# Kernel optimization log

Measured on AMD Instinct MI355X. Metric: run time of the kernel, lower is better.

The kernel has to match this reference:

```python
import jax, jax.numpy as jnp
import numpy as np


def setup_inputs() -> dict:
    key = jax.random.key(0)
    k1, k2, k3, k4 = jax.random.split(key, 4)
    b, N, c, h, w = 8, 150, 256, 128, 128
    mask_embed = jax.random.normal(k1, (b, N, c), dtype=jnp.float32)
    mask_features = jax.random.normal(k2, (b, c, h, w), dtype=jnp.float32)
    # Linear weights, torch convention: y = x @ W.T, std=0.02 trunc-normal-ish
    W_cls = jax.random.normal(k3, (c, c), dtype=jnp.float32) * 0.02
    W_feat = jax.random.normal(k4, (c, c), dtype=jnp.float32) * 0.02
    return {"mask_embed": mask_embed, "mask_features": mask_features,
            "W_cls": W_cls, "W_feat": W_feat}


def reference(mask_embed, mask_features, W_cls, W_feat):
    b, c, h, w = mask_features.shape
    cls_repr = mask_embed                                  # [b, N, c]
    img_feat = jnp.transpose(mask_features, (0, 2, 3, 1)).reshape(b, h * w, c)  # [b, hw, c]
    # coupled_attn: [b, N, hw]
    coupled_attn = jnp.einsum('bpc,bnc->bnp', img_feat, cls_repr)
    # class-direction softmax over pixels (dim=2)
    cls_attn = jax.nn.softmax(coupled_attn, axis=2)        # [b, N, hw]
    cls_offset = jnp.einsum('bnp,bpc->bnc', cls_attn, img_feat) @ W_cls.T
    aligned_cls_repr = cls_repr + cls_offset               # [b, N, c]
    # pixel-direction softmax over classes (dim=1)
    pos_attn = jax.nn.softmax(coupled_attn, axis=1)        # [b, N, hw]
    feat_offset = jnp.einsum('bnp,bnc->bpc', pos_attn, cls_repr) @ W_feat.T
    aligned_img_feat = img_feat + feat_offset              # [b, hw, c]
    aligned_img_feat = jnp.transpose(aligned_img_feat, (0, 2, 1)).reshape(b, c, h, w)
    return aligned_cls_repr, aligned_img_feat
```

## Files before the change

kernel.cpp:

```cpp
#include <hip/hip_runtime.h>

typedef unsigned short u16;
typedef __attribute__((ext_vector_type(8))) _Float16 f16x8;
typedef __attribute__((ext_vector_type(2))) _Float16 f16x2;
typedef __attribute__((ext_vector_type(4))) float f32x4;
typedef __attribute__((ext_vector_type(4))) unsigned short u16x4;
typedef __attribute__((ext_vector_type(8))) unsigned short u16x8;

#define MFMA16F __builtin_amdgcn_mfma_f32_16x16x32_f16

#define HW   16384
#define NCLS 150
#define NPAD 160
#define CDIM 256

#define FT_STRIDE 264
#define KC_STRIDE 72
#define FN_STRIDE 72
#define EP_STRIDE 72
#define W_STRIDE  168
#define CT_STRIDE 264

#define SO_FT   0
#define SO_CK   33792
#define SO_ROWM 56832
#define SO_ROWS 59392
#define SO_PMX  61952
#define SO_PZS  62464
#define SO_RZ   62976
#define SO_LDS  63232

#define O0_LDS  (NPAD*EP_STRIDE*2 + 128*FN_STRIDE*2)

#define WS_CLSF  0
#define WS_CLSWT 655360
#define WS_MG    2359296
#define WS_RZ    2364416
#define WS_WCF   2369536
#define WS_COMBT 2500608
#define WS_ROWP  3155968
#define WS_PART  3155968
#define WS_S     24127488

__device__ __forceinline__ u16 f2h(float f){ return __builtin_bit_cast(u16, (_Float16)f); }
__device__ __forceinline__ float h2f(u16 h){ return (float)__builtin_bit_cast(_Float16, h); }
__device__ __forceinline__ f16x2 shfl_h2(f16x2 v, int m){
  int x = __builtin_bit_cast(int, v);
  x = __shfl_xor(x, m);
  return __builtin_bit_cast(f16x2, x);
}

__global__ __launch_bounds__(256) void k0(const float* __restrict__ cls, const float* __restrict__ Wf,
                                          const float* __restrict__ Wc,
                                          u16* __restrict__ clsF, u16* __restrict__ clsWT,
                                          u16* __restrict__ WcF){
  int t = threadIdx.x;
  if (blockIdx.x >= 8*NPAD){
    int i = ((blockIdx.x - 8*NPAD)*256 + t)*4;
    f32x4 v = *(const f32x4*)&Wc[i];
    u16x4 o = {f2h(v[0]), f2h(v[1]), f2h(v[2]), f2h(v[3])};
    *(u16x4*)&WcF[i] = o;
    return;
  }
  int b = blockIdx.x / NPAD, n = blockIdx.x % NPAD;
  __shared__ float row[256];
  int bn = b*NPAD + n;
  if (n < NCLS){
    float v = cls[(b*NCLS + n)*CDIM + t];
    clsF[bn*CDIM + t] = f2h(v);
    row[t] = v;
    __syncthreads();
    float acc = 0.f;
    const float* wr = Wf + t*CDIM;
    #pragma unroll 4
    for (int c = 0; c < 256; c += 4){
      acc += row[c]*wr[c] + row[c+1]*wr[c+1] + row[c+2]*wr[c+2] + row[c+3]*wr[c+3];
    }
    clsWT[(b*CDIM + t)*NPAD + n] = f2h(acc);
  } else {
    clsF[bn*CDIM + t] = 0;
    clsWT[(b*CDIM + t)*NPAD + n] = 0;
  }
}

__global__ __launch_bounds__(512) void kSO1(const float* __restrict__ feat,
                                            const u16* __restrict__ clsF,
                                            const u16* __restrict__ clsWT,
                                            u16* __restrict__ Sg, float* __restrict__ rowP,
                                            float* __restrict__ out1){
  extern __shared__ char sm[];
  u16*  ftF  = (u16*)(sm + SO_FT);
  u16*  clsK = (u16*)(sm + SO_CK);
  u16*  E    = (u16*)(sm + SO_CK);
  float* rowM = (float*)(sm + SO_ROWM);
  float* rowS = (float*)(sm + SO_ROWS);
  float* pmx  = (float*)(sm + SO_PMX);
  float* pzs  = (float*)(sm + SO_PZS);
  float* rzL  = (float*)(sm + SO_RZ);

  int b = blockIdx.x & 7, tl = blockIdx.x >> 3, t = threadIdx.x;
  int p0 = tl*64;
  const float* featG = feat + (size_t)b*CDIM*HW;
  const u16* clsB  = clsF  + b*NPAD*CDIM;
  const u16* clsWB = clsWT + b*CDIM*NPAD;
  u16* Sb = Sg + (size_t)b*NPAD*HW;

  int lane = t & 63, wv = t >> 6;
  int l15 = lane & 15, lk = (lane >> 4) & 3;
  int nh = wv >> 2, pq = wv & 3;
  int nbase = nh*80;
  int col = pq*16 + l15;
  int cstrip = wv*32;

  {
    int p = t & 63, cg = t >> 6;
    #pragma unroll
    for (int i = 0; i < 8; ++i){
      int c0 = (i*8 + cg)*4;
      const float* g0 = featG + (size_t)c0*HW + p0 + p;
      float v0 = g0[0], v1 = g0[HW], v2 = g0[2*HW], v3 = g0[3*HW];
      u16x4 hv = {f2h(v0), f2h(v1), f2h(v2), f2h(v3)};
      *(u16x4*)&ftF[p*FT_STRIDE + c0] = hv;
    }
  }
  f32x4 acc[5];
  #pragma unroll
  for (int f = 0; f < 5; ++f) acc[f] = (f32x4){0.f,0.f,0.f,0.f};
  for (int kc = 0; kc < 4; ++kc){
    #pragma unroll
    for (int it = 0; it < 3; ++it){
      int idx = it*512 + t;
      if (idx < 1280){
        int n = idx >> 3, s8 = idx & 7;
        u16x8 v = *(const u16x8*)&clsB[n*CDIM + kc*64 + s8*8];
        *(u16x8*)&clsK[n*KC_STRIDE + s8*8] = v;
      }
    }
    __syncthreads();
    #pragma unroll
    for (int kb2 = 0; kb2 < 2; ++kb2){
      int kol = kb2*32 + lk*8;
      f16x8 bh = *(const f16x8*)&ftF[(pq*16 + l15)*FT_STRIDE + kc*64 + kol];
      #pragma unroll
      for (int f = 0; f < 5; ++f){
        f16x8 ah = *(const f16x8*)&clsK[(nbase + f*16 + l15)*KC_STRIDE + kol];
        acc[f] = MFMA16F(ah, bh, acc[f], 0, 0, 0);
      }
    }
    __syncthreads();
  }
  f16x8 aw0[5], aw1[5];
  #pragma unroll
  for (int kb = 0; kb < 5; ++kb){
    aw0[kb] = *(const f16x8*)&clsWB[(cstrip + l15)*NPAD + kb*32 + lk*8];
    aw1[kb] = *(const f16x8*)&clsWB[(cstrip + 16 + l15)*NPAD + kb*32 + lk*8];
  }
  #pragma unroll
  for (int kb = 0; kb < 5; ++kb){
    asm volatile("" :: "v"(aw0[kb]), "v"(aw1[kb]));
  }
  #pragma unroll
  for (int f = 0; f < 5; ++f){
    #pragma unroll
    for (int r = 0; r < 4; ++r){
      int n = nbase + f*16 + 4*lk + r;
      Sb[(size_t)n*HW + p0 + col] = f2h(acc[f][r]);
    }
  }
  #pragma unroll
  for (int f = 0; f < 5; ++f){
    #pragma unroll
    for (int rp = 0; rp < 2; ++rp){
      float v0 = acc[f][rp*2], v1 = acc[f][rp*2 + 1];
      f16x2 pm_ = {(_Float16)v0, (_Float16)v1};
      pm_ = __builtin_elementwise_max(pm_, shfl_h2(pm_, 1));
      pm_ = __builtin_elementwise_max(pm_, shfl_h2(pm_, 2));
      pm_ = __builtin_elementwise_max(pm_, shfl_h2(pm_, 4));
      pm_ = __builtin_elementwise_max(pm_, shfl_h2(pm_, 8));
      float m0 = (float)pm_[0], m1 = (float)pm_[1];
      f16x2 ps_ = {(_Float16)__expf(v0 - m0), (_Float16)__expf(v1 - m1)};
      ps_ = ps_ + shfl_h2(ps_, 1);
      ps_ = ps_ + shfl_h2(ps_, 2);
      ps_ = ps_ + shfl_h2(ps_, 4);
      ps_ = ps_ + shfl_h2(ps_, 8);
      if (l15 == f){
        int n0 = nbase + f*16 + 4*lk + rp*2;
        rowM[n0*4 + pq]       = m0;
        rowM[(n0 + 1)*4 + pq] = m1;
        rowS[n0*4 + pq]       = (float)ps_[0];
        rowS[(n0 + 1)*4 + pq] = (float)ps_[1];
      }
    }
  }
  {
    float pmax = -3.0e38f;
    #pragma unroll
    for (int f = 0; f < 5; ++f)
      #pragma unroll
      for (int r = 0; r < 4; ++r){
        int n = nbase + 16*f + 4*lk + r;
        if (n < NCLS) pmax = fmaxf(pmax, acc[f][r]);
      }
    pmax = fmaxf(pmax, __shfl_xor(pmax, 16));
    pmax = fmaxf(pmax, __shfl_xor(pmax, 32));
    if (lk == 0) pmx[nh*64 + col] = pmax;
  }
  __syncthreads();
  if (t < NPAD){
    float rm0 = rowM[t*4+0], rm1 = rowM[t*4+1], rm2 = rowM[t*4+2], rm3 = rowM[t*4+3];
    float msub = fmaxf(fmaxf(rm0, rm1), fmaxf(rm2, rm3));
    float l = rowS[t*4+0]*__expf(rm0 - msub) + rowS[t*4+1]*__expf(rm1 - msub)
            + rowS[t*4+2]*__expf(rm2 - msub) + rowS[t*4+3]*__expf(rm3 - msub);
    float* rp = rowP + ((size_t)(b*256 + tl)*NPAD + t)*2;
    rp[0] = msub;
    rp[1] = l;
  }
  {
    float mp_ = fmaxf(pmx[col], pmx[64 + col]);
    float s = 0.f;
    #pragma unroll
    for (int f = 0; f < 5; ++f){
      u16x4 ev;
      #pragma unroll
      for (int r = 0; r < 4; ++r){
        int n = nbase + 16*f + 4*lk + r;
        float e = (n < NCLS) ? __expf(acc[f][r] - mp_) : 0.f;
        s += e;
        ev[r] = f2h(e);
      }
      *(u16x4*)&E[col*W_STRIDE + nbase + 16*f + 4*lk] = ev;
    }
    s += __shfl_xor(s, 16);
    s += __shfl_xor(s, 32);
    if (lk == 0) pzs[nh*64 + col] = s;
  }
  __syncthreads();
  if (t < 64) rzL[t] = 1.0f / (pzs[t] + pzs[64 + t]);
  f32x4 accO[2][4];
  #pragma unroll
  for (int cf = 0; cf < 2; ++cf)
    #pragma unroll
    for (int pf = 0; pf < 4; ++pf) accO[cf][pf] = (f32x4){0.f,0.f,0.f,0.f};
  #pragma unroll
  for (int kb = 0; kb < 5; ++kb){
    int ko = kb*32 + lk*8;
    #pragma unroll
    for (int pf = 0; pf < 4; ++pf){
      f16x8 bb = *(const f16x8*)&E[(pf*16 + l15)*W_STRIDE + ko];
      accO[0][pf] = MFMA16F(aw0[kb], bb, accO[0][pf], 0, 0, 0);
      accO[1][pf] = MFMA16F(aw1[kb], bb, accO[1][pf], 0, 0, 0);
    }
  }
  __syncthreads();
  #pragma unroll
  for (int cf = 0; cf < 2; ++cf){
    #pragma unroll
    for (int r = 0; r < 4; ++r){
      int c = cstrip + cf*16 + lk*4 + r;
      float* ob = out1 + (size_t)(b*CDIM + c)*HW + p0;
      #pragma unroll
      for (int pf = 0; pf < 4; ++pf){
        int pp = pf*16 + l15;
        ob[pp] = accO[cf][pf][r]*rzL[pp] + h2f(ftF[pp*FT_STRIDE + c]);
      }
    }
  }
}

__global__ __launch_bounds__(256) void kComb(const float* __restrict__ rowP,
                                             float* __restrict__ mg, float* __restrict__ rz){
  int b = blockIdx.x / 10, nb = blockIdx.x % 10, t = threadIdx.x;
  int sg = t >> 4, j = t & 15;
  int n = nb*16 + j;
  __shared__ float pm[16][17], pl[16][17];
  float m = -3.0e38f, l = 0.f;
  for (int i = 0; i < 16; ++i){
    int s = sg*16 + i;
    const float* rp = rowP + ((size_t)(b*256 + s)*NPAD + n)*2;
    float ms = rp[0], ls = rp[1];
    float mn = fmaxf(m, ms);
    l = l*__expf(m - mn) + ls*__expf(ms - mn);
    m = mn;
  }
  pm[sg][j] = m;
  pl[sg][j] = l;
  __syncthreads();
  if (sg == 0){
    float M = pm[0][j], L = pl[0][j];
    #pragma unroll
    for (int k = 1; k < 16; ++k){
      float ms = pm[k][j], ls = pl[k][j];
      float mn = fmaxf(M, ms);
      L = L*__expf(M - mn) + ls*__expf(ms - mn);
      M = mn;
    }
    mg[b*NPAD + n] = M;
    rz[b*NPAD + n] = 1.0f / L;
  }
}

__global__ __launch_bounds__(512) void kOut0(const u16* __restrict__ Sg, const float* __restrict__ feat,
                                             const float* __restrict__ mg, u16* __restrict__ part){
  extern __shared__ char sm[];
  u16* Ep = (u16*)sm;
  u16* fN = (u16*)(sm + NPAD*EP_STRIDE*2);
  int b = blockIdx.x & 7, pr = (blockIdx.x >> 3) & 31, ch = (blockIdx.x >> 8) & 1;
  int t = threadIdx.x;
  const u16* Sb = Sg + (size_t)b*NPAD*HW;
  const float* featB = feat + (size_t)b*CDIM*HW;
  const float* mgB = mg + b*NPAD;
  int lane = t & 63, wv = t >> 6;
  int l15 = lane & 15, lk = (lane >> 4) & 3;
  int cstrip = wv*16;
  int rr = t >> 3, px8 = (t & 7)*8;
  f32x4 acc[10];
  #pragma unroll
  for (int nf = 0; nf < 10; ++nf) acc[nf] = (f32x4){0.f,0.f,0.f,0.f};
  for (int ck = 0; ck < 8; ++ck){
    int p0 = pr*512 + ck*64;
    #pragma unroll
    for (int ps = 0; ps < 3; ++ps){
      int rowi = ps*64 + rr;
      if (rowi < NPAD){
        u16x8 v = *(const u16x8*)&Sb[(size_t)rowi*HW + p0 + px8];
        float m = mgB[rowi];
        u16x8 o;
        #pragma unroll
        for (int j = 0; j < 8; ++j) o[j] = f2h(__expf(h2f(v[j]) - m));
        *(u16x8*)&Ep[rowi*EP_STRIDE + px8] = o;
      }
    }
    #pragma unroll
    for (int ps = 0; ps < 2; ++ps){
      int cl = ps*64 + rr;
      const float* g = featB + (size_t)(ch*128 + cl)*HW + p0 + px8;
      f32x4 v0 = *(const f32x4*)&g[0];
      f32x4 v1 = *(const f32x4*)&g[4];
      u16x8 o = {f2h(v0[0]), f2h(v0[1]), f2h(v0[2]), f2h(v0[3]),
                 f2h(v1[0]), f2h(v1[1]), f2h(v1[2]), f2h(v1[3])};
      *(u16x8*)&fN[cl*FN_STRIDE + px8] = o;
    }
    __syncthreads();
    #pragma unroll
    for (int kb = 0; kb < 2; ++kb){
      int ko = kb*32 + lk*8;
      f16x8 a0 = *(const f16x8*)&fN[(cstrip + l15)*FN_STRIDE + ko];
      #pragma unroll
      for (int nf = 0; nf < 10; ++nf){
        f16x8 bb = *(const f16x8*)&Ep[(nf*16 + l15)*EP_STRIDE + ko];
        acc[nf] = MFMA16F(a0, bb, acc[nf], 0, 0, 0);
      }
    }
    __syncthreads();
  }
  #pragma unroll
  for (int nf = 0; nf < 10; ++nf){
    #pragma unroll
    for (int r = 0; r < 4; ++r){
      int c = ch*128 + cstrip + lk*4 + r;
      int n = nf*16 + l15;
      part[((size_t)(b*32 + pr)*CDIM + c)*NPAD + n] = f2h(acc[nf][r]);
    }
  }
}

__global__ __launch_bounds__(256) void k4a(const u16* __restrict__ part, const float* __restrict__ rz,
                                           u16* __restrict__ combT){
  int b = blockIdx.x / 20, sub = blockIdx.x % 20, t = threadIdx.x;
  int idx8 = (sub*256 + t)*8;
  int c = idx8 / NPAD, n0 = idx8 % NPAD;
  const u16* base = part + (size_t)(b*32)*CDIM*NPAD + idx8;
  float a[8];
  #pragma unroll
  for (int j = 0; j < 8; ++j) a[j] = 0.f;
  for (int s = 0; s < 32; ++s){
    u16x8 v = *(const u16x8*)&base[(size_t)s*CDIM*NPAD];
    #pragma unroll
    for (int j = 0; j < 8; ++j) a[j] += h2f(v[j]);
  }
  const float* rzB = rz + b*NPAD + n0;
  #pragma unroll
  for (int j = 0; j < 8; ++j){
    combT[((size_t)(b*NPAD) + n0 + j)*CDIM + c] = f2h(a[j] * rzB[j]);
  }
}

__global__ __launch_bounds__(512) void k4b(const u16* __restrict__ combT, const u16* __restrict__ WcF,
                                           const float* __restrict__ cls, float* __restrict__ out0){
  extern __shared__ char sm[];
  u16* A = (u16*)sm;
  int b = blockIdx.x >> 1, nb = blockIdx.x & 1, t = threadIdx.x;
  const u16* cb = combT + (size_t)(b*NPAD + nb*80)*CDIM;
  #pragma unroll
  for (int it = 0; it < 10; ++it){
    int idx8 = (it*512 + t)*8;
    if (idx8 < 80*256){
      int row = idx8 >> 8, k0 = idx8 & 255;
      u16x8 v = *(const u16x8*)&cb[idx8];
      *(u16x8*)&A[row*CT_STRIDE + k0] = v;
    }
  }
  __syncthreads();
  int lane = t & 63, wv = t >> 6;
  int l15 = lane & 15, lk = (lane >> 4) & 3;
  int cstrip = wv*32;
  f32x4 acc[5][2];
  #pragma unroll
  for (int f = 0; f < 5; ++f)
    #pragma unroll
    for (int ct = 0; ct < 2; ++ct) acc[f][ct] = (f32x4){0.f,0.f,0.f,0.f};
  #pragma unroll
  for (int kb = 0; kb < 8; ++kb){
    int ko = kb*32 + lk*8;
    f16x8 b0 = *(const f16x8*)&WcF[(cstrip + l15)*CDIM + ko];
    f16x8 b1 = *(const f16x8*)&WcF[(cstrip + 16 + l15)*CDIM + ko];
    #pragma unroll
    for (int f = 0; f < 5; ++f){
      f16x8 af = *(const f16x8*)&A[(f*16 + l15)*CT_STRIDE + ko];
      acc[f][0] = MFMA16F(af, b0, acc[f][0], 0, 0, 0);
      acc[f][1] = MFMA16F(af, b1, acc[f][1], 0, 0, 0);
    }
  }
  #pragma unroll
  for (int f = 0; f < 5; ++f){
    #pragma unroll
    for (int r = 0; r < 4; ++r){
      int n = nb*80 + f*16 + lk*4 + r;
      if (n < NCLS){
        #pragma unroll
        for (int ct = 0; ct < 2; ++ct){
          int c = cstrip + ct*16 + l15;
          out0[(size_t)(b*NCLS + n)*CDIM + c] = cls[(size_t)(b*NCLS + n)*CDIM + c] + acc[f][ct][r];
        }
      }
    }
  }
}

extern "C" void kernel_launch(void* const* d_in, const int* in_sizes, int n_in,
                              void* d_out, int out_size, void* d_ws, size_t ws_size,
                              hipStream_t stream){
  (void)in_sizes; (void)n_in; (void)out_size; (void)ws_size;
  const float* cls  = (const float*)d_in[0];
  const float* feat = (const float*)d_in[1];
  const float* Wc   = (const float*)d_in[2];
  const float* Wf   = (const float*)d_in[3];
  float* out0 = (float*)d_out;
  float* out1 = out0 + 8*NCLS*CDIM;
  char* ws = (char*)d_ws;
  u16*   clsF   = (u16*)(ws + WS_CLSF);
  u16*   clsWT  = (u16*)(ws + WS_CLSWT);
  float* mgv    = (float*)(ws + WS_MG);
  float* rzv    = (float*)(ws + WS_RZ);
  u16*   WcFv   = (u16*)(ws + WS_WCF);
  u16*   combTv = (u16*)(ws + WS_COMBT);
  float* rowPv  = (float*)(ws + WS_ROWP);
  u16*   partv  = (u16*)(ws + WS_PART);
  u16*   Sgp    = (u16*)(ws + WS_S);

  (void)hipFuncSetAttribute((const void*)kSO1, hipFuncAttributeMaxDynamicSharedMemorySize, SO_LDS);

  k0   <<<8*NPAD + 64, 256, 0, stream>>>(cls, Wf, Wc, clsF, clsWT, WcFv);
  kSO1 <<<2048, 512, SO_LDS, stream>>>(feat, clsF, clsWT, Sgp, rowPv, out1);
  kComb<<<80, 256, 0, stream>>>(rowPv, mgv, rzv);
  kOut0<<<512, 512, O0_LDS, stream>>>(Sgp, feat, mgv, partv);
  k4a  <<<160, 256, 0, stream>>>(partv, rzv, combTv);
  k4b  <<<16, 512, 80*CT_STRIDE*2, stream>>>(combTv, WcFv, cls, out0);
}
```

Baseline: 195.2 us.

## Make kSO1 persistent over four pixel tiles with resident class matrix and prefetch

```diff
diff --git a/kernel.cpp b/kernel.cpp
--- a/kernel.cpp
+++ b/kernel.cpp
@@ -15,20 +15,21 @@
 #define CDIM 256
 
 #define FT_STRIDE 264
-#define KC_STRIDE 72
+#define CL_STRIDE 264
 #define FN_STRIDE 72
 #define EP_STRIDE 72
 #define W_STRIDE  168
 #define CT_STRIDE 264
 
-#define SO_FT   0
-#define SO_CK   33792
-#define SO_ROWM 56832
-#define SO_ROWS 59392
-#define SO_PMX  61952
-#define SO_PZS  62464
-#define SO_RZ   62976
-#define SO_LDS  63232
+#define SO_CL   0
+#define SO_FT   84480
+#define SO_E    118272
+#define SO_ROWM 139776
+#define SO_ROWS 142336
+#define SO_PMX  144896
+#define SO_PZS  145408
+#define SO_RZ   145920
+#define SO_LDS  146176
 
 #define O0_LDS  (NPAD*EP_STRIDE*2 + 128*FN_STRIDE*2)
 
@@ -89,17 +90,16 @@
                                             u16* __restrict__ Sg, float* __restrict__ rowP,
                                             float* __restrict__ out1){
   extern __shared__ char sm[];
+  u16*  clsL = (u16*)(sm + SO_CL);
   u16*  ftF  = (u16*)(sm + SO_FT);
-  u16*  clsK = (u16*)(sm + SO_CK);
-  u16*  E    = (u16*)(sm + SO_CK);
+  u16*  E    = (u16*)(sm + SO_E);
   float* rowM = (float*)(sm + SO_ROWM);
   float* rowS = (float*)(sm + SO_ROWS);
   float* pmx  = (float*)(sm + SO_PMX);
   float* pzs  = (float*)(sm + SO_PZS);
   float* rzL  = (float*)(sm + SO_RZ);
 
-  int b = blockIdx.x & 7, tl = blockIdx.x >> 3, t = threadIdx.x;
-  int p0 = tl*64;
+  int b = blockIdx.x & 7, ch = blockIdx.x >> 3, t = threadIdx.x;
   const float* featG = feat + (size_t)b*CDIM*HW;
   const u16* clsB  = clsF  + b*NPAD*CDIM;
   const u16* clsWB = clsWT + b*CDIM*NPAD;
@@ -111,43 +111,14 @@
   int nbase = nh*80;
   int col = pq*16 + l15;
   int cstrip = wv*32;
-
-  {
-    int p = t & 63, cg = t >> 6;
-    #pragma unroll
-    for (int i = 0; i < 8; ++i){
-      int c0 = (i*8 + cg)*4;
-      const float* g0 = featG + (size_t)c0*HW + p0 + p;
-      float v0 = g0[0], v1 = g0[HW], v2 = g0[2*HW], v3 = g0[3*HW];
-      u16x4 hv = {f2h(v0), f2h(v1), f2h(v2), f2h(v3)};
-      *(u16x4*)&ftF[p*FT_STRIDE + c0] = hv;
-    }
-  }
-  f32x4 acc[5];
-  #pragma unroll
-  for (int f = 0; f < 5; ++f) acc[f] = (f32x4){0.f,0.f,0.f,0.f};
-  for (int kc = 0; kc < 4; ++kc){
-    #pragma unroll
-    for (int it = 0; it < 3; ++it){
-      int idx = it*512 + t;
-      if (idx < 1280){
-        int n = idx >> 3, s8 = idx & 7;
-        u16x8 v = *(const u16x8*)&clsB[n*CDIM + kc*64 + s8*8];
-        *(u16x8*)&clsK[n*KC_STRIDE + s8*8] = v;
-      }
-    }
-    __syncthreads();
-    #pragma unroll
-    for (int kb2 = 0; kb2 < 2; ++kb2){
-      int kol = kb2*32 + lk*8;
-      f16x8 bh = *(const f16x8*)&ftF[(pq*16 + l15)*FT_STRIDE + kc*64 + kol];
-      #pragma unroll
-      for (int f = 0; f < 5; ++f){
-        f16x8 ah = *(const f16x8*)&clsK[(nbase + f*16 + l15)*KC_STRIDE + kol];
-        acc[f] = MFMA16F(ah, bh, acc[f], 0, 0, 0);
-      }
-    }
-    __syncthreads();
+  int p = t & 63, cg = t >> 6;
+
+  #pragma unroll
+  for (int it = 0; it < 10; ++it){
+    int idx8 = (it*512 + t)*8;
+    int n = idx8 >> 8, c = idx8 & 255;
+    u16x8 v = *(const u16x8*)&clsB[idx8];
+    *(u16x8*)&clsL[n*CL_STRIDE + c] = v;
   }
   f16x8 aw0[5], aw1[5];
   #pragma unroll
@@ -159,109 +130,153 @@
   for (int kb = 0; kb < 5; ++kb){
     asm volatile("" :: "v"(aw0[kb]), "v"(aw1[kb]));
   }
-  #pragma unroll
-  for (int f = 0; f < 5; ++f){
-    #pragma unroll
-    for (int r = 0; r < 4; ++r){
-      int n = nbase + f*16 + 4*lk + r;
-      Sb[(size_t)n*HW + p0 + col] = f2h(acc[f][r]);
-    }
-  }
-  #pragma unroll
-  for (int f = 0; f < 5; ++f){
-    #pragma unroll
-    for (int rp = 0; rp < 2; ++rp){
-      float v0 = acc[f][rp*2], v1 = acc[f][rp*2 + 1];
-      f16x2 pm_ = {(_Float16)v0, (_Float16)v1};
-      pm_ = __builtin_elementwise_max(pm_, shfl_h2(pm_, 1));
-      pm_ = __builtin_elementwise_max(pm_, shfl_h2(pm_, 2));
-      pm_ = __builtin_elementwise_max(pm_, shfl_h2(pm_, 4));
-      pm_ = __builtin_elementwise_max(pm_, shfl_h2(pm_, 8));
-      float m0 = (float)pm_[0], m1 = (float)pm_[1];
-      f16x2 ps_ = {(_Float16)__expf(v0 - m0), (_Float16)__expf(v1 - m1)};
-      ps_ = ps_ + shfl_h2(ps_, 1);
-      ps_ = ps_ + shfl_h2(ps_, 2);
-      ps_ = ps_ + shfl_h2(ps_, 4);
-      ps_ = ps_ + shfl_h2(ps_, 8);
-      if (l15 == f){
-        int n0 = nbase + f*16 + 4*lk + rp*2;
-        rowM[n0*4 + pq]       = m0;
-        rowM[(n0 + 1)*4 + pq] = m1;
-        rowS[n0*4 + pq]       = (float)ps_[0];
-        rowS[(n0 + 1)*4 + pq] = (float)ps_[1];
-      }
-    }
-  }
+  f32x4 pf[8];
   {
-    float pmax = -3.0e38f;
-    #pragma unroll
-    for (int f = 0; f < 5; ++f)
+    int p00 = ch*256;
+    #pragma unroll
+    for (int i = 0; i < 8; ++i){
+      int c0 = (i*8 + cg)*4;
+      const float* g0 = featG + (size_t)c0*HW + p00 + p;
+      pf[i][0] = g0[0]; pf[i][1] = g0[HW]; pf[i][2] = g0[2*HW]; pf[i][3] = g0[3*HW];
+    }
+  }
+
+  for (int tl = 0; tl < 4; ++tl){
+    int p0 = ch*256 + tl*64;
+    __syncthreads();
+    #pragma unroll
+    for (int i = 0; i < 8; ++i){
+      int c0 = (i*8 + cg)*4;
+      u16x4 hv = {f2h(pf[i][0]), f2h(pf[i][1]), f2h(pf[i][2]), f2h(pf[i][3])};
+      *(u16x4*)&ftF[p*FT_STRIDE + c0] = hv;
+    }
+    if (tl < 3){
+      int p0n = p0 + 64;
+      #pragma unroll
+      for (int i = 0; i < 8; ++i){
+        int c0 = (i*8 + cg)*4;
+        const float* g0 = featG + (size_t)c0*HW + p0n + p;
+        pf[i][0] = g0[0]; pf[i][1] = g0[HW]; pf[i][2] = g0[2*HW]; pf[i][3] = g0[3*HW];
+      }
+    }
+    __syncthreads();
+    f32x4 acc[5];
+    #pragma unroll
+    for (int f = 0; f < 5; ++f) acc[f] = (f32x4){0.f,0.f,0.f,0.f};
+    #pragma unroll
+    for (int kb = 0; kb < 8; ++kb){
+      int ko = kb*32 + lk*8;
+      f16x8 bh = *(const f16x8*)&ftF[(pq*16 + l15)*FT_STRIDE + ko];
+      #pragma unroll
+      for (int f = 0; f < 5; ++f){
+        f16x8 ah = *(const f16x8*)&clsL[(nbase + f*16 + l15)*CL_STRIDE + ko];
+        acc[f] = MFMA16F(ah, bh, acc[f], 0, 0, 0);
+      }
+    }
+    #pragma unroll
+    for (int f = 0; f < 5; ++f){
       #pragma unroll
       for (int r = 0; r < 4; ++r){
-        int n = nbase + 16*f + 4*lk + r;
-        if (n < NCLS) pmax = fmaxf(pmax, acc[f][r]);
-      }
-    pmax = fmaxf(pmax, __shfl_xor(pmax, 16));
-    pmax = fmaxf(pmax, __shfl_xor(pmax, 32));
-    if (lk == 0) pmx[nh*64 + col] = pmax;
-  }
-  __syncthreads();
-  if (t < NPAD){
-    float rm0 = rowM[t*4+0], rm1 = rowM[t*4+1], rm2 = rowM[t*4+2], rm3 = rowM[t*4+3];
-    float msub = fmaxf(fmaxf(rm0, rm1), fmaxf(rm2, rm3));
-    float l = rowS[t*4+0]*__expf(rm0 - msub) + rowS[t*4+1]*__expf(rm1 - msub)
-            + rowS[t*4+2]*__expf(rm2 - msub) + rowS[t*4+3]*__expf(rm3 - msub);
-    float* rp = rowP + ((size_t)(b*256 + tl)*NPAD + t)*2;
-    rp[0] = msub;
-    rp[1] = l;
-  }
-  {
-    float mp_ = fmaxf(pmx[col], pmx[64 + col]);
-    float s = 0.f;
+        int n = nbase + f*16 + 4*lk + r;
+        Sb[(size_t)n*HW + p0 + col] = f2h(acc[f][r]);
+      }
+    }
     #pragma unroll
     for (int f = 0; f < 5; ++f){
-      u16x4 ev;
+      #pragma unroll
+      for (int rp = 0; rp < 2; ++rp){
+        float v0 = acc[f][rp*2], v1 = acc[f][rp*2 + 1];
+        f16x2 pm_ = {(_Float16)v0, (_Float16)v1};
+        pm_ = __builtin_elementwise_max(pm_, shfl_h2(pm_, 1));
+        pm_ = __builtin_elementwise_max(pm_, shfl_h2(pm_, 2));
+        pm_ = __builtin_elementwise_max(pm_, shfl_h2(pm_, 4));
+        pm_ = __builtin_elementwise_max(pm_, shfl_h2(pm_, 8));
+        float m0 = (float)pm_[0], m1 = (float)pm_[1];
+        f16x2 ps_ = {(_Float16)__expf(v0 - m0), (_Float16)__expf(v1 - m1)};
+        ps_ = ps_ + shfl_h2(ps_, 1);
+        ps_ = ps_ + shfl_h2(ps_, 2);
+        ps_ = ps_ + shfl_h2(ps_, 4);
+        ps_ = ps_ + shfl_h2(ps_, 8);
+        if (l15 == f){
+          int n0 = nbase + f*16 + 4*lk + rp*2;
+          rowM[n0*4 + pq]       = m0;
+          rowM[(n0 + 1)*4 + pq] = m1;
+          rowS[n0*4 + pq]       = (float)ps_[0];
+          rowS[(n0 + 1)*4 + pq] = (float)ps_[1];
+        }
+      }
+    }
+    {
+      float pmax = -3.0e38f;
+      #pragma unroll
+      for (int f = 0; f < 5; ++f)
+        #pragma unroll
+        for (int r = 0; r < 4; ++r){
+          int n = nbase + 16*f + 4*lk + r;
+          if (n < NCLS) pmax = fmaxf(pmax, acc[f][r]);
+        }
+      pmax = fmaxf(pmax, __shfl_xor(pmax, 16));
+      pmax = fmaxf(pmax, __shfl_xor(pmax, 32));
+      if (lk == 0) pmx[nh*64 + col] = pmax;
+    }
+    __syncthreads();
+    if (t < NPAD){
+      float rm0 = rowM[t*4+0], rm1 = rowM[t*4+1], rm2 = rowM[t*4+2], rm3 = rowM[t*4+3];
+      float msub = fmaxf(fmaxf(rm0, rm1), fmaxf(rm2, rm3));
+      float l = rowS[t*4+0]*__expf(rm0 - msub) + rowS[t*4+1]*__expf(rm1 - msub)
+              + rowS[t*4+2]*__expf(rm2 - msub) + rowS[t*4+3]*__expf(rm3 - msub);
+      float* rp = rowP + ((size_t)(b*256 + ch*4 + tl)*NPAD + t)*2;
+      rp[0] = msub;
+      rp[1] = l;
+    }
+    {
+      float mp_ = fmaxf(pmx[col], pmx[64 + col]);
+      float s = 0.f;
+      #pragma unroll
+      for (int f = 0; f < 5; ++f){
+        u16x4 ev;
+        #pragma unroll
+        for (int r = 0; r < 4; ++r){
+          int n = nbase + 16*f + 4*lk + r;
+          float e = (n < NCLS) ? __expf(acc[f][r] - mp_) : 0.f;
+          s += e;
+          ev[r] = f2h(e);
+        }
+        *(u16x4*)&E[col*W_STRIDE + nbase + 16*f + 4*lk] = ev;
+      }
+      s += __shfl_xor(s, 16);
+      s += __shfl_xor(s, 32);
+      if (lk == 0) pzs[nh*64 + col] = s;
+    }
+    __syncthreads();
+    if (t < 64) rzL[t] = 1.0f / (pzs[t] + pzs[64 + t]);
+    f32x4 accO[2][4];
+    #pragma unroll
+    for (int cf = 0; cf < 2; ++cf)
+      #pragma unroll
+      for (int pfi = 0; pfi < 4; ++pfi) accO[cf][pfi] = (f32x4){0.f,0.f,0.f,0.f};
+    #pragma unroll
+    for (int kb = 0; kb < 5; ++kb){
+      int ko = kb*32 + lk*8;
+      #pragma unroll
+      for (int pfi = 0; pfi < 4; ++pfi){
+        f16x8 bb = *(const f16x8*)&E[(pfi*16 + l15)*W_STRIDE + ko];
+        accO[0][pfi] = MFMA16F(aw0[kb], bb, accO[0][pfi], 0, 0, 0);
+        accO[1][pfi] = MFMA16F(aw1[kb], bb, accO[1][pfi], 0, 0, 0);
+      }
+    }
+    __syncthreads();
+    #pragma unroll
+    for (int cf = 0; cf < 2; ++cf){
       #pragma unroll
       for (int r = 0; r < 4; ++r){
-        int n = nbase + 16*f + 4*lk + r;
-        float e = (n < NCLS) ? __expf(acc[f][r] - mp_) : 0.f;
-        s += e;
-        ev[r] = f2h(e);
-      }
-      *(u16x4*)&E[col*W_STRIDE + nbase + 16*f + 4*lk] = ev;
-    }
-    s += __shfl_xor(s, 16);
-    s += __shfl_xor(s, 32);
-    if (lk == 0) pzs[nh*64 + col] = s;
-  }
-  __syncthreads();
-  if (t < 64) rzL[t] = 1.0f / (pzs[t] + pzs[64 + t]);
-  f32x4 accO[2][4];
-  #pragma unroll
-  for (int cf = 0; cf < 2; ++cf)
-    #pragma unroll
-    for (int pf = 0; pf < 4; ++pf) accO[cf][pf] = (f32x4){0.f,0.f,0.f,0.f};
-  #pragma unroll
-  for (int kb = 0; kb < 5; ++kb){
-    int ko = kb*32 + lk*8;
-    #pragma unroll
-    for (int pf = 0; pf < 4; ++pf){
-      f16x8 bb = *(const f16x8*)&E[(pf*16 + l15)*W_STRIDE + ko];
-      accO[0][pf] = MFMA16F(aw0[kb], bb, accO[0][pf], 0, 0, 0);
-      accO[1][pf] = MFMA16F(aw1[kb], bb, accO[1][pf], 0, 0, 0);
-    }
-  }
-  __syncthreads();
-  #pragma unroll
-  for (int cf = 0; cf < 2; ++cf){
-    #pragma unroll
-    for (int r = 0; r < 4; ++r){
-      int c = cstrip + cf*16 + lk*4 + r;
-      float* ob = out1 + (size_t)(b*CDIM + c)*HW + p0;
-      #pragma unroll
-      for (int pf = 0; pf < 4; ++pf){
-        int pp = pf*16 + l15;
-        ob[pp] = accO[cf][pf][r]*rzL[pp] + h2f(ftF[pp*FT_STRIDE + c]);
+        int c = cstrip + cf*16 + lk*4 + r;
+        float* ob = out1 + (size_t)(b*CDIM + c)*HW + p0;
+        #pragma unroll
+        for (int pfi = 0; pfi < 4; ++pfi){
+          int pp = pfi*16 + l15;
+          ob[pp] = accO[cf][pfi][r]*rzL[pp] + h2f(ftF[pp*FT_STRIDE + c]);
+        }
       }
     }
   }
@@ -461,7 +476,7 @@
   (void)hipFuncSetAttribute((const void*)kSO1, hipFuncAttributeMaxDynamicSharedMemorySize, SO_LDS);
 
   k0   <<<8*NPAD + 64, 256, 0, stream>>>(cls, Wf, Wc, clsF, clsWT, WcFv);
-  kSO1 <<<2048, 512, SO_LDS, stream>>>(feat, clsF, clsWT, Sgp, rowPv, out1);
+  kSO1 <<<512, 512, SO_LDS, stream>>>(feat, clsF, clsWT, Sgp, rowPv, out1);
   kComb<<<80, 256, 0, stream>>>(rowPv, mgv, rzv);
   kOut0<<<512, 512, O0_LDS, stream>>>(Sgp, feat, mgv, partv);
   k4a  <<<160, 256, 0, stream>>>(partv, rzv, combTv);
```

After: 192.3 us. About the same (-1.5%).
